# Kernel optimization log

Hardware: AMD Instinct MI355X
Metric: run time of the kernel (lower is better)

Reference implementation:

```python
import jax, jax.numpy as jnp
import numpy as np

N_BINS = 15


def setup_inputs() -> dict:
    key = jax.random.key(0)
    k1, k2 = jax.random.split(key)
    N, C = 262144, 1000
    logits = jax.random.normal(k1, (N, C), dtype=jnp.float32)
    labels = jax.random.randint(k2, (N,), 0, C, dtype=jnp.int64)
    return {"logits": logits, "labels": labels}


def reference(logits, labels):
    # softmax + max over classes -> per-sample confidence and prediction
    probs = jax.nn.softmax(logits, axis=1)
    confidences = jnp.max(probs, axis=1)            # [N]
    predictions = jnp.argmax(probs, axis=1)         # [N]
    accuracies = (predictions == labels).astype(confidences.dtype)

    # Bin b covers (b/n_bins, (b+1)/n_bins]  (lower exclusive, upper inclusive),
    # matching conf > lower & conf <= upper: bin = ceil(conf*n_bins) - 1.
    bin_idx = jnp.clip(
        jnp.ceil(confidences * N_BINS).astype(jnp.int32) - 1, 0, N_BINS - 1
    )

    n = confidences.shape[0]
    counts = jax.ops.segment_sum(jnp.ones_like(confidences), bin_idx, num_segments=N_BINS)
    conf_sum = jax.ops.segment_sum(confidences, bin_idx, num_segments=N_BINS)
    acc_sum = jax.ops.segment_sum(accuracies, bin_idx, num_segments=N_BINS)

    safe = jnp.maximum(counts, 1.0)
    avg_conf = conf_sum / safe
    avg_acc = acc_sum / safe
    prop = counts / n
    ece = jnp.sum(jnp.where(counts > 0, jnp.abs(avg_conf - avg_acc) * prop, 0.0))
    return ece
```

## Files before the change

kernel.cpp:

```cpp
#include <hip/hip_runtime.h>
#include <math.h>
#include <limits.h>

#define NBINS 15

typedef float f32x4 __attribute__((ext_vector_type(4)));

__global__ void ece_zero_ws(float* ws) {
    int i = threadIdx.x;
    if (i < NBINS * 3) ws[i] = 0.0f;
}

template <int NV>
__global__ void __launch_bounds__(256, 4) ece_main_reg(
    const float* __restrict__ logits, const int* __restrict__ labels,
    float* __restrict__ ws, int N, int C) {
    __shared__ float lds[NBINS * 3];
    if (threadIdx.x < NBINS * 3) lds[threadIdx.x] = 0.0f;
    __syncthreads();

    const int lane = threadIdx.x & 63;
    const int wid  = blockIdx.x * (blockDim.x >> 6) + (threadIdx.x >> 6);
    const int nw   = gridDim.x * (blockDim.x >> 6);
    const int nvec = C >> 2;

    for (int row = wid; row < N; row += nw) {
        const f32x4* rp = (const f32x4*)(logits + (size_t)row * (size_t)C);

        f32x4 r[NV];
        #pragma unroll
        for (int j = 0; j < NV; ++j) {
            int idx = lane + j * 64;
            if (idx < nvec) {
                r[j] = __builtin_nontemporal_load(&rp[idx]);
            } else {
                r[j] = (f32x4){-INFINITY, -INFINITY, -INFINITY, -INFINITY};
            }
        }

        float m = -INFINITY;
        #pragma unroll
        for (int j = 0; j < NV; ++j) {
            m = fmaxf(m, fmaxf(fmaxf(r[j].x, r[j].y), fmaxf(r[j].z, r[j].w)));
        }
        #pragma unroll
        for (int off = 32; off >= 1; off >>= 1)
            m = fmaxf(m, __shfl_xor(m, off));

        float s = 0.0f;
        int   mi = INT_MAX;
        #pragma unroll
        for (int j = 0; j < NV; ++j) {
            int gi = (lane + j * 64) << 2;
            float ex = __expf(r[j].x - m);
            float ey = __expf(r[j].y - m);
            float ez = __expf(r[j].z - m);
            float ew = __expf(r[j].w - m);
            s += (ex + ey) + (ez + ew);
            if (r[j].x == m) mi = min(mi, gi);
            if (r[j].y == m) mi = min(mi, gi + 1);
            if (r[j].z == m) mi = min(mi, gi + 2);
            if (r[j].w == m) mi = min(mi, gi + 3);
        }
        #pragma unroll
        for (int off = 32; off >= 1; off >>= 1) {
            s += __shfl_xor(s, off);
            mi = min(mi, __shfl_xor(mi, off));
        }

        if (lane == 0) {
            float conf = 1.0f / s;
            float acc  = (labels[row] == mi) ? 1.0f : 0.0f;
            int b = (int)ceilf(conf * (float)NBINS) - 1;
            b = b < 0 ? 0 : (b > NBINS - 1 ? NBINS - 1 : b);
            atomicAdd(&lds[b * 3 + 0], 1.0f);
            atomicAdd(&lds[b * 3 + 1], conf);
            atomicAdd(&lds[b * 3 + 2], acc);
        }
    }

    __syncthreads();
    if (threadIdx.x < NBINS * 3) atomicAdd(&ws[threadIdx.x], lds[threadIdx.x]);
}

__global__ void __launch_bounds__(256, 4) ece_main_gen(
    const float* __restrict__ logits, const int* __restrict__ labels,
    float* __restrict__ ws, int N, int C) {
    __shared__ float lds[NBINS * 3];
    if (threadIdx.x < NBINS * 3) lds[threadIdx.x] = 0.0f;
    __syncthreads();

    const int lane = threadIdx.x & 63;
    const int wid  = blockIdx.x * (blockDim.x >> 6) + (threadIdx.x >> 6);
    const int nw   = gridDim.x * (blockDim.x >> 6);

    for (int row = wid; row < N; row += nw) {
        const float* rp = logits + (size_t)row * (size_t)C;
        float m = -INFINITY;
        float s = 0.0f;
        int   mi = INT_MAX;
        for (int i = lane; i < C; i += 64) {
            float v = rp[i];
            if (v > m) { s = s * __expf(m - v) + 1.0f; m = v; mi = i; }
            else       { s += __expf(v - m); }
        }
        #pragma unroll
        for (int off = 32; off >= 1; off >>= 1) {
            float om  = __shfl_xor(m, off);
            float os  = __shfl_xor(s, off);
            int   omi = __shfl_xor(mi, off);
            float nm  = fmaxf(m, om);
            float e1  = (m  > -INFINITY) ? __expf(m  - nm) : 0.0f;
            float e2  = (om > -INFINITY) ? __expf(om - nm) : 0.0f;
            s = s * e1 + os * e2;
            if (om > m || (om == m && omi < mi)) mi = omi;
            m = nm;
        }
        if (lane == 0) {
            float conf = 1.0f / s;
            float acc  = (labels[row] == mi) ? 1.0f : 0.0f;
            int b = (int)ceilf(conf * (float)NBINS) - 1;
            b = b < 0 ? 0 : (b > NBINS - 1 ? NBINS - 1 : b);
            atomicAdd(&lds[b * 3 + 0], 1.0f);
            atomicAdd(&lds[b * 3 + 1], conf);
            atomicAdd(&lds[b * 3 + 2], acc);
        }
    }

    __syncthreads();
    if (threadIdx.x < NBINS * 3) atomicAdd(&ws[threadIdx.x], lds[threadIdx.x]);
}

__global__ void ece_final(const float* __restrict__ ws, float* __restrict__ out, float n) {
    if (threadIdx.x == 0) {
        float ece = 0.0f;
        #pragma unroll
        for (int b = 0; b < NBINS; ++b) {
            float c  = ws[b * 3 + 0];
            float cs = ws[b * 3 + 1];
            float as = ws[b * 3 + 2];
            if (c > 0.0f) ece += fabsf(cs / c - as / c) * (c / n);
        }
        out[0] = ece;
    }
}

extern "C" void kernel_launch(void* const* d_in, const int* in_sizes, int n_in,
                              void* d_out, int out_size, void* d_ws, size_t ws_size,
                              hipStream_t stream) {
    const float* logits = (const float*)d_in[0];
    const int*   labels = (const int*)d_in[1];
    float* out = (float*)d_out;
    float* ws  = (float*)d_ws;

    const int N = in_sizes[1];
    const int C = in_sizes[0] / in_sizes[1];

    ece_zero_ws<<<1, 64, 0, stream>>>(ws);

    const int threads = 256;
    int blocks = (N + (threads / 64) - 1) / (threads / 64);
    if (blocks > 2048) blocks = 2048;

    if ((C & 3) == 0 && C <= 4 * 64 * 4) {
        ece_main_reg<4><<<blocks, threads, 0, stream>>>(logits, labels, ws, N, C);
    } else if ((C & 3) == 0 && C <= 8 * 64 * 4) {
        ece_main_reg<8><<<blocks, threads, 0, stream>>>(logits, labels, ws, N, C);
    } else {
        ece_main_gen<<<blocks, threads, 0, stream>>>(logits, labels, ws, N, C);
    }

    ece_final<<<1, 64, 0, stream>>>(ws, out, (float)N);
}
```

Measured before the change: 185.3 us.

## Double-buffer row loads in register softmax kernel with contiguous row chunks

Each wave now owns a contiguous chunk of rows instead of a grid-strided set. It loads the next row into a second register buffer while it computes the current one, so global load latency overlaps the reductions. This doubles the per-row register footprint (NV=4 gives 32 extra VGPRs), which could limit occupancy under the launch bounds, and contiguous chunks change the DRAM access pattern across waves.

```diff
diff --git a/kernel.cpp b/kernel.cpp
--- a/kernel.cpp
+++ b/kernel.cpp
@@ -24,25 +24,27 @@
     const int nw   = gridDim.x * (blockDim.x >> 6);
     const int nvec = C >> 2;
 
-    for (int row = wid; row < N; row += nw) {
+    const int rpw  = (N + nw - 1) / nw;
+    const int row0 = wid * rpw;
+    const int row1 = (row0 + rpw < N) ? (row0 + rpw) : N;
+
+    f32x4 bufA[NV], bufB[NV];
+
+    auto load_row = [&](int row, f32x4 (&r)[NV]) {
         const f32x4* rp = (const f32x4*)(logits + (size_t)row * (size_t)C);
-
-        f32x4 r[NV];
         #pragma unroll
         for (int j = 0; j < NV; ++j) {
             int idx = lane + j * 64;
-            if (idx < nvec) {
-                r[j] = __builtin_nontemporal_load(&rp[idx]);
-            } else {
-                r[j] = (f32x4){-INFINITY, -INFINITY, -INFINITY, -INFINITY};
-            }
+            if (idx < nvec) r[j] = __builtin_nontemporal_load(&rp[idx]);
+            else            r[j] = (f32x4){-INFINITY, -INFINITY, -INFINITY, -INFINITY};
         }
+    };
 
+    auto compute_row = [&](int row, f32x4 (&r)[NV]) {
         float m = -INFINITY;
         #pragma unroll
-        for (int j = 0; j < NV; ++j) {
+        for (int j = 0; j < NV; ++j)
             m = fmaxf(m, fmaxf(fmaxf(r[j].x, r[j].y), fmaxf(r[j].z, r[j].w)));
-        }
         #pragma unroll
         for (int off = 32; off >= 1; off >>= 1)
             m = fmaxf(m, __shfl_xor(m, off));
@@ -76,6 +78,21 @@
             atomicAdd(&lds[b * 3 + 0], 1.0f);
             atomicAdd(&lds[b * 3 + 1], conf);
             atomicAdd(&lds[b * 3 + 2], acc);
+        }
+    };
+
+    if (row0 < row1) {
+        load_row(row0, bufA);
+        int row = row0;
+        for (;;) {
+            if (row + 1 < row1) load_row(row + 1, bufB);
+            compute_row(row, bufA);
+            ++row;
+            if (row >= row1) break;
+            if (row + 1 < row1) load_row(row + 1, bufA);
+            compute_row(row, bufB);
+            ++row;
+            if (row >= row1) break;
         }
     }
 
```

Result: slower. 194.9 us (+5.2%).
